# Performance work log

Hardware: AMD Instinct MI355X
Metric: run time of the kernel (lower is better)

## Reference

```python
import jax, jax.numpy as jnp
import numpy as np

EPS = 0.3
LAYERS = 2


def setup_inputs() -> dict:
    key = jax.random.key(0)
    ks = jax.random.split(key, 8)
    N, F, H, C, E = 50000, 512, 128, 40, 800000

    def xavier(k, shape):
        fan_out, fan_in = shape[0], shape[-1]
        std = 1.414 * np.sqrt(2.0 / (fan_in + fan_out))
        return (jax.random.normal(k, shape, jnp.float32) * std).astype(jnp.float32)

    return {
        "x": jax.random.normal(ks[0], (N, F), jnp.float32),
        "t1_w": xavier(ks[1], (H, F)),
        "t1_b": jnp.zeros((H,), jnp.float32),
        "t2_w": xavier(ks[2], (C, H)),
        "t2_b": jnp.zeros((C,), jnp.float32),
        "gate_w": xavier(ks[3], (LAYERS, 2 * H)),  # Linear(2H,1) weight per layer
        "gate_b": jnp.zeros((LAYERS,), jnp.float32),
        "edge_index": jax.random.randint(ks[4], (2, E), 0, N, jnp.int32),
    }


def reference(x, t1_w, t1_b, t2_w, t2_b, gate_w, gate_b, edge_index):
    N = x.shape[0]
    H = t1_w.shape[0]
    row, col = edge_index[0], edge_index[1]  # source, target

    # norm_degree = degree(row).clamp(min=1) ** -0.5
    deg = jax.ops.segment_sum(jnp.ones_like(row, dtype=x.dtype), row, num_segments=N)
    nd = jnp.clip(deg, 1.0) ** -0.5  # [N]
    nd_r, nd_c = nd[row], nd[col]    # [E]

    # dropout is identity in eval mode
    h = jax.nn.relu(x @ t1_w.T + t1_b)  # [N,H]
    raw = h
    for l in range(LAYERS):
        h_src = h[row]  # x_j, [E,H]
        h_dst = h[col]  # [E,H]
        # gate(cat([h[row], h[col]])) == h_src @ W[:H] + h_dst @ W[H:] + b
        g = jnp.tanh(h_src @ gate_w[l, :H] + h_dst @ gate_w[l, H:] + gate_b[l])  # [E]
        norm = g * nd_r * nd_c  # [E]
        agg = jax.ops.segment_sum(norm[:, None] * h_src, col, num_segments=N)  # scatter-add at targets
        h = EPS * raw + agg
    out = h @ t2_w.T + t2_b  # [N,C]
    return jax.nn.log_softmax(out, axis=1)
```

## Files before the change

kernel.cpp:

```cpp
#include <hip/hip_runtime.h>
#include <math.h>

#define F_DIM 512
#define H_DIM 128
#define C_DIM 40
#define EPS_F 0.3f
#define NBLK 160

typedef float f32x4 __attribute__((ext_vector_type(4)));
typedef unsigned int u32x4 __attribute__((ext_vector_type(4)));
typedef __bf16 bf16x8 __attribute__((ext_vector_type(8)));
typedef unsigned long long u64;
typedef unsigned short ushort_t;

__device__ inline float bflo(unsigned t) { return __builtin_bit_cast(float, t << 16); }
__device__ inline float bfhi(unsigned t) { return __builtin_bit_cast(float, t & 0xffff0000u); }
__device__ inline unsigned short f2bf(float f) {
  unsigned u = __builtin_bit_cast(unsigned, f);
  u = (u + 0x7fffu + ((u >> 16) & 1u)) >> 16;
  return (unsigned short)u;
}
__device__ inline unsigned pack2bf(float a, float b) {
  unsigned ua = __builtin_bit_cast(unsigned, a);
  unsigned ub = __builtin_bit_cast(unsigned, b);
  ua = (ua + 0x7fffu + ((ua >> 16) & 1u)) >> 16;
  ub = (ub + 0x7fffu + ((ub >> 16) & 1u)) >> 16;
  return ua | (ub << 16);
}


__global__ __launch_bounds__(256) void part_count(const int* __restrict__ row,
    const int* __restrict__ col, int* __restrict__ blkhist, int E, int nbkt, int chunk) {
  __shared__ int ch[256], rh[256];
  int t = threadIdx.x, b = blockIdx.x;
  ch[t] = 0; rh[t] = 0;
  __syncthreads();
  int s = b * chunk, e = min(E, s + chunk);
  for (int i = s + t; i < e; i += 256) {
    atomicAdd(&ch[((unsigned)col[i]) >> 8], 1);
    atomicAdd(&rh[((unsigned)row[i]) >> 8], 1);
  }
  __syncthreads();
  if (t < nbkt) {
    blkhist[t * NBLK + b] = ch[t];
    blkhist[nbkt * NBLK + t * NBLK + b] = rh[t];
  }
}

__global__ __launch_bounds__(256) void scan_partial(const int* __restrict__ cnt,
    int* __restrict__ part, int M) {
  __shared__ int sd[256];
  int t = threadIdx.x;
  int i = blockIdx.x * 256 + t;
  sd[t] = (i < M) ? cnt[i] : 0;
  __syncthreads();
  for (int s = 128; s > 0; s >>= 1) {
    if (t < s) sd[t] += sd[t + s];
    __syncthreads();
  }
  if (t == 0) part[blockIdx.x] = sd[0];
}

__global__ __launch_bounds__(256) void scan_single(int* __restrict__ part, int P) {
  __shared__ int sd[256];
  int t = threadIdx.x;
  sd[t] = (t < P) ? part[t] : 0;
  __syncthreads();
  for (int off = 1; off < 256; off <<= 1) {
    int add = (t >= off) ? sd[t - off] : 0;
    __syncthreads();
    sd[t] += add;
    __syncthreads();
  }
  if (t < P) part[t] = (t == 0) ? 0 : sd[t - 1];
}

__global__ __launch_bounds__(256) void scan_apply(const int* __restrict__ cnt,
    const int* __restrict__ part, int* __restrict__ sc, int M) {
  __shared__ int sd[256];
  int t = threadIdx.x;
  int i = blockIdx.x * 256 + t;
  int v = (i < M) ? cnt[i] : 0;
  sd[t] = v;
  __syncthreads();
  for (int off = 1; off < 256; off <<= 1) {
    int add = (t >= off) ? sd[t - off] : 0;
    __syncthreads();
    sd[t] += add;
    __syncthreads();
  }
  if (i < M) {
    int excl = (t == 0) ? 0 : sd[t - 1];
    sc[i] = part[blockIdx.x] + excl;
  }
}

__global__ __launch_bounds__(256) void part_scatter(const int* __restrict__ row,
    const int* __restrict__ col, const int* __restrict__ sc,
    u64* __restrict__ colpart, int* __restrict__ rowpart, int E, int nbkt, int chunk) {
  __shared__ int cbase[256], rbase[256], coff[256], roff[256];
  int t = threadIdx.x, b = blockIdx.x;
  if (t < nbkt) {
    cbase[t] = sc[t * NBLK + b];
    rbase[t] = sc[nbkt * NBLK + t * NBLK + b] - E;
  }
  coff[t] = 0; roff[t] = 0;
  __syncthreads();
  int s = b * chunk, e = min(E, s + chunk);
  for (int i = s + t; i < e; i += 256) {
    unsigned c = (unsigned)col[i], r = (unsigned)row[i];
    int pc = cbase[c >> 8] + atomicAdd(&coff[c >> 8], 1);
    colpart[pc] = ((u64)r << 32) | (u64)c;
    int pr = rbase[r >> 8] + atomicAdd(&roff[r >> 8], 1);
    rowpart[pr] = (int)r;
  }
}

__global__ __launch_bounds__(256) void bucket_csr(const u64* __restrict__ colpart,
    const int* __restrict__ sc, int* __restrict__ col_ptr, int* __restrict__ csr_src,
    int N, int E, int nbkt) {
  __shared__ int cnt[256], ex[256], off[256];
  int t = threadIdx.x, bkt = blockIdx.x;
  int s = sc[bkt * NBLK];
  int e = sc[(bkt + 1) * NBLK];
  cnt[t] = 0; off[t] = 0;
  __syncthreads();
  for (int i = s + t; i < e; i += 256)
    atomicAdd(&cnt[(int)(colpart[i] & 255u)], 1);
  __syncthreads();
  ex[t] = cnt[t];
  __syncthreads();
  for (int o = 1; o < 256; o <<= 1) {
    int v = (t >= o) ? ex[t - o] : 0;
    __syncthreads();
    ex[t] += v;
    __syncthreads();
  }
  int excl = (t == 0) ? 0 : ex[t - 1];
  __syncthreads();
  ex[t] = excl;
  __syncthreads();
  int node = bkt * 256 + t;
  if (node < N) col_ptr[node] = s + ex[t];
  if (bkt == 0 && t == 0) col_ptr[N] = E;
  for (int i = s + t; i < e; i += 256) {
    u64 p = colpart[i];
    int lb = (int)(p & 255u);
    int dst = s + ex[lb] + atomicAdd(&off[lb], 1);
    csr_src[dst] = (int)(p >> 32);
  }
}

__global__ __launch_bounds__(256) void bucket_deg(const int* __restrict__ rowpart,
    const int* __restrict__ sc, float* __restrict__ nd, int N, int E, int nbkt) {
  __shared__ int cnt[256];
  int t = threadIdx.x, bkt = blockIdx.x;
  int s = sc[nbkt * NBLK + bkt * NBLK] - E;
  int e = (bkt < nbkt - 1) ? (sc[nbkt * NBLK + (bkt + 1) * NBLK] - E) : E;
  cnt[t] = 0;
  __syncthreads();
  for (int i = s + t; i < e; i += 256)
    atomicAdd(&cnt[rowpart[i] & 255], 1);
  __syncthreads();
  int node = bkt * 256 + t;
  if (node < N) {
    int d = cnt[t] < 1 ? 1 : cnt[t];
    nd[node] = 1.0f / sqrtf((float)d);
  }
}


__global__ __launch_bounds__(256) void gemm1_mfma(const float* __restrict__ x,
    const float* __restrict__ w, const float* __restrict__ b,
    ushort_t* __restrict__ hbf, int N) {
  __shared__ u32x4 AsBuf[512];
  __shared__ u32x4 BsBuf[1024];
  char* Asc = (char*)AsBuf;
  char* Bsc = (char*)BsBuf;

  int t = threadIdx.x;
  int lane = t & 63;
  int wid = t >> 6;
  int wm = wid >> 1;
  int wn = wid & 1;
  int m0 = blockIdx.x * 64;

  f32x4 acc[2][4];
#pragma unroll
  for (int i = 0; i < 2; ++i)
#pragma unroll
    for (int j = 0; j < 4; ++j) acc[i][j] = (f32x4){0.f, 0.f, 0.f, 0.f};

  float bias[4];
#pragma unroll
  for (int j = 0; j < 4; ++j) bias[j] = b[wn * 64 + j * 16 + (lane & 15)];

  for (int kk = 0; kk < F_DIM; kk += 64) {
#pragma unroll
    for (int q = 0; q < 2; ++q) {
      int c = q * 256 + t;
      int row = c >> 3, kc = c & 7;
      int gm = m0 + row;
      f32x4 v0 = {0.f, 0.f, 0.f, 0.f}, v1 = {0.f, 0.f, 0.f, 0.f};
      if (gm < N) {
        const float* src = &x[(size_t)gm * F_DIM + kk + kc * 8];
        v0 = *(const f32x4*)src;
        v1 = *(const f32x4*)(src + 4);
      }
      u32x4 pk;
      pk[0] = pack2bf(v0[0], v0[1]);
      pk[1] = pack2bf(v0[2], v0[3]);
      pk[2] = pack2bf(v1[0], v1[1]);
      pk[3] = pack2bf(v1[2], v1[3]);
      *(u32x4*)(Asc + row * 128 + ((kc ^ (row & 7)) << 4)) = pk;
    }
#pragma unroll
    for (int q = 0; q < 4; ++q) {
      int c = q * 256 + t;
      int row = c >> 3, kc = c & 7;
      const float* src = &w[(size_t)row * F_DIM + kk + kc * 8];
      f32x4 v0 = *(const f32x4*)src;
      f32x4 v1 = *(const f32x4*)(src + 4);
      u32x4 pk;
      pk[0] = pack2bf(v0[0], v0[1]);
      pk[1] = pack2bf(v0[2], v0[3]);
      pk[2] = pack2bf(v1[0], v1[1]);
      pk[3] = pack2bf(v1[2], v1[3]);
      *(u32x4*)(Bsc + row * 128 + ((kc ^ (row & 7)) << 4)) = pk;
    }
    __syncthreads();
#pragma unroll
    for (int kh = 0; kh < 2; ++kh) {
      bf16x8 af[2], bfr[4];
      int kc = kh * 4 + (lane >> 4);
#pragma unroll
      for (int i = 0; i < 2; ++i) {
        int row = wm * 32 + i * 16 + (lane & 15);
        af[i] = *(const bf16x8*)(Asc + row * 128 + ((kc ^ (row & 7)) << 4));
      }
#pragma unroll
      for (int j = 0; j < 4; ++j) {
        int row = wn * 64 + j * 16 + (lane & 15);
        bfr[j] = *(const bf16x8*)(Bsc + row * 128 + ((kc ^ (row & 7)) << 4));
      }
#pragma unroll
      for (int i = 0; i < 2; ++i)
#pragma unroll
        for (int j = 0; j < 4; ++j)
          acc[i][j] = __builtin_amdgcn_mfma_f32_16x16x32_bf16(af[i], bfr[j], acc[i][j], 0, 0, 0);
    }
    __syncthreads();
  }

#pragma unroll
  for (int i = 0; i < 2; ++i)
#pragma unroll
    for (int j = 0; j < 4; ++j) {
      int col = wn * 64 + j * 16 + (lane & 15);
      int rbase = m0 + wm * 32 + i * 16 + ((lane >> 4) * 4);
#pragma unroll
      for (int r = 0; r < 4; ++r) {
        int gr = rbase + r;
        if (gr < N) hbf[(size_t)gr * H_DIM + col] = f2bf(fmaxf(acc[i][j][r] + bias[j], 0.f));
      }
    }
}


__global__ __launch_bounds__(256) void gate_s(const ushort_t* __restrict__ hbf,
    const float* __restrict__ gwl, const float* __restrict__ gb, int layer,
    float* __restrict__ s1, float* __restrict__ s2, int N) {
  int wid = (blockIdx.x * 256 + threadIdx.x) >> 6;
  int lane = threadIdx.x & 63;
  if (wid >= N) return;
  unsigned tv = *(const unsigned*)&hbf[(size_t)wid * H_DIM + lane * 2];
  float hx = bflo(tv), hy = bfhi(tv);
  float2 g1 = *(const float2*)&gwl[lane * 2];
  float2 g2 = *(const float2*)&gwl[H_DIM + lane * 2];
  float p1 = hx * g1.x + hy * g1.y;
  float p2 = hx * g2.x + hy * g2.y;
  for (int off = 32; off > 0; off >>= 1) {
    p1 += __shfl_xor(p1, off);
    p2 += __shfl_xor(p2, off);
  }
  if (lane == 0) {
    s1[wid] = p1;
    s2[wid] = p2 + gb[layer];
  }
}


__global__ __launch_bounds__(256) void agg_kernel(const ushort_t* __restrict__ hbf,
    const ushort_t* __restrict__ rawbf, const float* __restrict__ s1,
    const float* __restrict__ s2pb, const float* __restrict__ nd,
    const int* __restrict__ col_ptr, const int* __restrict__ csr_src,
    ushort_t* __restrict__ houtbf, int N) {
  int wid = (blockIdx.x * 256 + threadIdx.x) >> 6;
  int lane = threadIdx.x & 63;
  if (wid >= N) return;
  int v = wid;
  int p0 = col_ptr[v], p1 = col_ptr[v + 1];
  float s2v = s2pb[v];
  float ndv = nd[v];
  float ax = 0.f, ay = 0.f;
  for (int base = p0; base < p1; base += 64) {
    int idx = base + lane;
    int u = 0;
    float cf = 0.f;
    if (idx < p1) {
      u = csr_src[idx];
      cf = tanhf(s1[u] + s2v) * nd[u] * ndv;
    }
    int cnt = p1 - base;
    if (cnt > 64) cnt = 64;
    int j = 0;
    for (; j + 4 <= cnt; j += 4) {
      int u0 = __shfl(u, j + 0), u1 = __shfl(u, j + 1);
      int u2 = __shfl(u, j + 2), u3 = __shfl(u, j + 3);
      float c0 = __shfl(cf, j + 0), c1 = __shfl(cf, j + 1);
      float c2 = __shfl(cf, j + 2), c3 = __shfl(cf, j + 3);
      unsigned t0 = *(const unsigned*)&hbf[(size_t)u0 * H_DIM + lane * 2];
      unsigned t1 = *(const unsigned*)&hbf[(size_t)u1 * H_DIM + lane * 2];
      unsigned t2 = *(const unsigned*)&hbf[(size_t)u2 * H_DIM + lane * 2];
      unsigned t3 = *(const unsigned*)&hbf[(size_t)u3 * H_DIM + lane * 2];
      ax += c0 * bflo(t0) + c1 * bflo(t1) + c2 * bflo(t2) + c3 * bflo(t3);
      ay += c0 * bfhi(t0) + c1 * bfhi(t1) + c2 * bfhi(t2) + c3 * bfhi(t3);
    }
    for (; j < cnt; ++j) {
      int uj = __shfl(u, j);
      float cj = __shfl(cf, j);
      unsigned tj = *(const unsigned*)&hbf[(size_t)uj * H_DIM + lane * 2];
      ax += cj * bflo(tj);
      ay += cj * bfhi(tj);
    }
  }
  unsigned rv = *(const unsigned*)&rawbf[(size_t)v * H_DIM + lane * 2];
  float ox = EPS_F * bflo(rv) + ax;
  float oy = EPS_F * bfhi(rv) + ay;
  *(unsigned*)&houtbf[(size_t)v * H_DIM + lane * 2] = pack2bf(ox, oy);
}


__global__ __launch_bounds__(256) void gemm2_lsm(const ushort_t* __restrict__ hbf,
    const float* __restrict__ w, const float* __restrict__ b,
    float* __restrict__ out, int N) {
  __shared__ float ws[C_DIM][129];
  __shared__ float bsh[C_DIM];
  __shared__ float hsm[4][H_DIM];
  int t = threadIdx.x;
  for (int i = t; i < C_DIM * H_DIM; i += 256) ws[i / H_DIM][i % H_DIM] = w[i];
  if (t < C_DIM) bsh[t] = b[t];
  __syncthreads();
  int wave = t >> 6, lane = t & 63;
  for (int vb = blockIdx.x * 4; vb < N; vb += gridDim.x * 4) {
    int v = vb + wave;
    bool act = v < N;
    if (act) {
      unsigned hv = *(const unsigned*)&hbf[(size_t)v * H_DIM + lane * 2];
      hsm[wave][lane * 2] = bflo(hv);
      hsm[wave][lane * 2 + 1] = bfhi(hv);
    }
    __syncthreads();
    float acc = 0.f;
    if (act && lane < C_DIM) {
#pragma unroll 8
      for (int k = 0; k < H_DIM; ++k)
        acc = fmaf(hsm[wave][k], ws[lane][k], acc);
      acc += bsh[lane];
    }
    float m = (lane < C_DIM) ? acc : -1e30f;
    for (int off = 32; off > 0; off >>= 1) m = fmaxf(m, __shfl_xor(m, off));
    float ex = (lane < C_DIM) ? expf(acc - m) : 0.f;
    float s = ex;
    for (int off = 32; off > 0; off >>= 1) s += __shfl_xor(s, off);
    float lse = m + logf(s);
    if (act && lane < C_DIM) out[(size_t)v * C_DIM + lane] = acc - lse;
    __syncthreads();
  }
}


extern "C" void kernel_launch(void* const* d_in, const int* in_sizes, int n_in,
                              void* d_out, int out_size, void* d_ws, size_t ws_size,
                              hipStream_t stream) {
  const float* x   = (const float*)d_in[0];
  const float* t1w = (const float*)d_in[1];
  const float* t1b = (const float*)d_in[2];
  const float* t2w = (const float*)d_in[3];
  const float* t2b = (const float*)d_in[4];
  const float* gw  = (const float*)d_in[5];
  const float* gb  = (const float*)d_in[6];
  const int*   ei  = (const int*)d_in[7];
  const int N = in_sizes[0] / F_DIM;
  const int E = in_sizes[7] / 2;
  float* out = (float*)d_out;

  char* p = (char*)d_ws;
  auto take = [&](size_t bytes) {
    char* r = p;
    p += (bytes + 255) & ~(size_t)255;
    return r;
  };
  ushort_t* h0 = (ushort_t*)take((size_t)N * H_DIM * 2);
  ushort_t* h1 = (ushort_t*)take((size_t)N * H_DIM * 2);
  ushort_t* h2 = (ushort_t*)take((size_t)N * H_DIM * 2);
  float* s1 = (float*)take((size_t)N * 4);
  float* s2 = (float*)take((size_t)N * 4);
  float* nd = (float*)take((size_t)N * 4);
  int* col_ptr = (int*)take((size_t)(N + 1) * 4);
  int* csr_src = (int*)take((size_t)E * 4);

  const int nbkt = (N + 255) >> 8;
  const int chunk = (E + NBLK - 1) / NBLK;
  const int M = 2 * nbkt * NBLK;
  const int scanblocks = (M + 255) / 256;

  int* blkhist = (int*)take((size_t)M * 4);
  int* sc      = (int*)take((size_t)M * 4);
  int* part    = (int*)take(256 * 4);
  u64* colpart = (u64*)take((size_t)E * 8);
  int* rowpart = (int*)take((size_t)E * 4);

  const int* row = ei;
  const int* col = ei + E;

  part_count<<<NBLK, 256, 0, stream>>>(row, col, blkhist, E, nbkt, chunk);
  scan_partial<<<scanblocks, 256, 0, stream>>>(blkhist, part, M);
  scan_single<<<1, 256, 0, stream>>>(part, scanblocks);
  scan_apply<<<scanblocks, 256, 0, stream>>>(blkhist, part, sc, M);
  part_scatter<<<NBLK, 256, 0, stream>>>(row, col, sc, colpart, rowpart, E, nbkt, chunk);
  bucket_csr<<<nbkt, 256, 0, stream>>>(colpart, sc, col_ptr, csr_src, N, E, nbkt);
  bucket_deg<<<nbkt, 256, 0, stream>>>(rowpart, sc, nd, N, E, nbkt);

  gemm1_mfma<<<(N + 63) / 64, 256, 0, stream>>>(x, t1w, t1b, h0, N);

  int nwb = (N + 3) / 4;
  gate_s<<<nwb, 256, 0, stream>>>(h0, gw + 0 * 2 * H_DIM, gb, 0, s1, s2, N);
  agg_kernel<<<nwb, 256, 0, stream>>>(h0, h0, s1, s2, nd, col_ptr, csr_src, h1, N);
  gate_s<<<nwb, 256, 0, stream>>>(h1, gw + 1 * 2 * H_DIM, gb, 1, s1, s2, N);
  agg_kernel<<<nwb, 256, 0, stream>>>(h1, h0, s1, s2, nd, col_ptr, csr_src, h2, N);

  gemm2_lsm<<<1024, 256, 0, stream>>>(h2, t2w, t2b, out, N);
}
```

Measured before the change: 218.4 us.

## Fuse CSR build scans, compact partitions, enlarge GEMM1 tile, fuse gate into aggregation

The three-kernel global scan goes away: each part_scatter block computes its own bucket offsets by scanning the block histogram redundantly. Partitions shrink to 32-bit col and 8-bit row entries, and the CSR and degree bucket kernels merge into one launch. GEMM1 now processes 128 rows per block with a larger A tile, and the second layer's gate scores are computed in the first aggregation kernel's epilogue so the second gate_s launch is dropped. The redundant per-block histogram scan adds work to every block, and packing the row as r<<8 in 32 bits assumes fewer than 2^24 nodes.

```diff
diff --git a/kernel.cpp b/kernel.cpp
--- a/kernel.cpp
+++ b/kernel.cpp
@@ -5,13 +5,13 @@
 #define H_DIM 128
 #define C_DIM 40
 #define EPS_F 0.3f
-#define NBLK 160
+#define NBLK 256
 
 typedef float f32x4 __attribute__((ext_vector_type(4)));
 typedef unsigned int u32x4 __attribute__((ext_vector_type(4)));
 typedef __bf16 bf16x8 __attribute__((ext_vector_type(8)));
-typedef unsigned long long u64;
 typedef unsigned short ushort_t;
+typedef unsigned char uchar_t;
 
 __device__ inline float bflo(unsigned t) { return __builtin_bit_cast(float, t << 16); }
 __device__ inline float bfhi(unsigned t) { return __builtin_bit_cast(float, t & 0xffff0000u); }
@@ -43,129 +43,111 @@
   __syncthreads();
   if (t < nbkt) {
     blkhist[t * NBLK + b] = ch[t];
-    blkhist[nbkt * NBLK + t * NBLK + b] = rh[t];
-  }
-}
-
-__global__ __launch_bounds__(256) void scan_partial(const int* __restrict__ cnt,
-    int* __restrict__ part, int M) {
-  __shared__ int sd[256];
-  int t = threadIdx.x;
-  int i = blockIdx.x * 256 + t;
-  sd[t] = (i < M) ? cnt[i] : 0;
-  __syncthreads();
-  for (int s = 128; s > 0; s >>= 1) {
-    if (t < s) sd[t] += sd[t + s];
-    __syncthreads();
-  }
-  if (t == 0) part[blockIdx.x] = sd[0];
-}
-
-__global__ __launch_bounds__(256) void scan_single(int* __restrict__ part, int P) {
-  __shared__ int sd[256];
-  int t = threadIdx.x;
-  sd[t] = (t < P) ? part[t] : 0;
+    blkhist[(nbkt + t) * NBLK + b] = rh[t];
+  }
+}
+
+__global__ __launch_bounds__(256) void part_scatter(const int* __restrict__ row,
+    const int* __restrict__ col, const int* __restrict__ blkhist,
+    int* __restrict__ bktbase, unsigned* __restrict__ colpart,
+    uchar_t* __restrict__ rowpart, int E, int nbkt, int chunk) {
+  __shared__ int sbase[400];
+  __shared__ int stot[400];
+  __shared__ int psum[256];
+  __shared__ int sc[400];
+  __shared__ int coff[400];
+  int t = threadIdx.x, b = blockIdx.x;
+  int nrows = 2 * nbkt;
+  for (int rr = t; rr < nrows; rr += 256) {
+    const int* rp = &blkhist[rr * NBLK];
+    int pre = 0, tot = 0;
+    for (int i = 0; i < NBLK; ++i) {
+      int v = rp[i];
+      pre += (i < b) ? v : 0;
+      tot += v;
+    }
+    sbase[rr] = pre; stot[rr] = tot;
+  }
+  __syncthreads();
+  int e0 = (2 * t     < nrows) ? stot[2 * t]     : 0;
+  int e1 = (2 * t + 1 < nrows) ? stot[2 * t + 1] : 0;
+  psum[t] = e0 + e1;
   __syncthreads();
   for (int off = 1; off < 256; off <<= 1) {
-    int add = (t >= off) ? sd[t - off] : 0;
-    __syncthreads();
-    sd[t] += add;
-    __syncthreads();
-  }
-  if (t < P) part[t] = (t == 0) ? 0 : sd[t - 1];
-}
-
-__global__ __launch_bounds__(256) void scan_apply(const int* __restrict__ cnt,
-    const int* __restrict__ part, int* __restrict__ sc, int M) {
-  __shared__ int sd[256];
-  int t = threadIdx.x;
-  int i = blockIdx.x * 256 + t;
-  int v = (i < M) ? cnt[i] : 0;
-  sd[t] = v;
-  __syncthreads();
-  for (int off = 1; off < 256; off <<= 1) {
-    int add = (t >= off) ? sd[t - off] : 0;
-    __syncthreads();
-    sd[t] += add;
-    __syncthreads();
-  }
-  if (i < M) {
-    int excl = (t == 0) ? 0 : sd[t - 1];
-    sc[i] = part[blockIdx.x] + excl;
-  }
-}
-
-__global__ __launch_bounds__(256) void part_scatter(const int* __restrict__ row,
-    const int* __restrict__ col, const int* __restrict__ sc,
-    u64* __restrict__ colpart, int* __restrict__ rowpart, int E, int nbkt, int chunk) {
-  __shared__ int cbase[256], rbase[256], coff[256], roff[256];
-  int t = threadIdx.x, b = blockIdx.x;
-  if (t < nbkt) {
-    cbase[t] = sc[t * NBLK + b];
-    rbase[t] = sc[nbkt * NBLK + t * NBLK + b] - E;
-  }
-  coff[t] = 0; roff[t] = 0;
+    int add = (t >= off) ? psum[t - off] : 0;
+    __syncthreads();
+    psum[t] += add;
+    __syncthreads();
+  }
+  int pex = (t == 0) ? 0 : psum[t - 1];
+  if (2 * t < nrows)     sc[2 * t]     = pex + sbase[2 * t];
+  if (2 * t + 1 < nrows) sc[2 * t + 1] = pex + e0 + sbase[2 * t + 1];
+  if (b == 0) {
+    if (2 * t < nrows)     bktbase[2 * t]     = pex;
+    if (2 * t + 1 < nrows) bktbase[2 * t + 1] = pex + e0;
+    if (t == 0) bktbase[nrows] = 2 * E;
+  }
+  for (int rr = t; rr < nrows; rr += 256) coff[rr] = 0;
   __syncthreads();
   int s = b * chunk, e = min(E, s + chunk);
   for (int i = s + t; i < e; i += 256) {
     unsigned c = (unsigned)col[i], r = (unsigned)row[i];
-    int pc = cbase[c >> 8] + atomicAdd(&coff[c >> 8], 1);
-    colpart[pc] = ((u64)r << 32) | (u64)c;
-    int pr = rbase[r >> 8] + atomicAdd(&roff[r >> 8], 1);
-    rowpart[pr] = (int)r;
-  }
-}
-
-__global__ __launch_bounds__(256) void bucket_csr(const u64* __restrict__ colpart,
-    const int* __restrict__ sc, int* __restrict__ col_ptr, int* __restrict__ csr_src,
+    int bc = (int)(c >> 8), br = (int)(r >> 8);
+    int pc = sc[bc] + atomicAdd(&coff[bc], 1);
+    colpart[pc] = (r << 8) | (c & 255u);
+    int pr = sc[nbkt + br] + atomicAdd(&coff[nbkt + br], 1) - E;
+    rowpart[pr] = (uchar_t)(r & 255u);
+  }
+}
+
+__global__ __launch_bounds__(256) void bucket_both(const unsigned* __restrict__ colpart,
+    const uchar_t* __restrict__ rowpart, const int* __restrict__ bktbase,
+    int* __restrict__ col_ptr, int* __restrict__ csr_src, float* __restrict__ nd,
     int N, int E, int nbkt) {
   __shared__ int cnt[256], ex[256], off[256];
-  int t = threadIdx.x, bkt = blockIdx.x;
-  int s = sc[bkt * NBLK];
-  int e = sc[(bkt + 1) * NBLK];
-  cnt[t] = 0; off[t] = 0;
-  __syncthreads();
-  for (int i = s + t; i < e; i += 256)
-    atomicAdd(&cnt[(int)(colpart[i] & 255u)], 1);
-  __syncthreads();
-  ex[t] = cnt[t];
-  __syncthreads();
-  for (int o = 1; o < 256; o <<= 1) {
-    int v = (t >= o) ? ex[t - o] : 0;
-    __syncthreads();
-    ex[t] += v;
-    __syncthreads();
-  }
-  int excl = (t == 0) ? 0 : ex[t - 1];
-  __syncthreads();
-  ex[t] = excl;
-  __syncthreads();
-  int node = bkt * 256 + t;
-  if (node < N) col_ptr[node] = s + ex[t];
-  if (bkt == 0 && t == 0) col_ptr[N] = E;
-  for (int i = s + t; i < e; i += 256) {
-    u64 p = colpart[i];
-    int lb = (int)(p & 255u);
-    int dst = s + ex[lb] + atomicAdd(&off[lb], 1);
-    csr_src[dst] = (int)(p >> 32);
-  }
-}
-
-__global__ __launch_bounds__(256) void bucket_deg(const int* __restrict__ rowpart,
-    const int* __restrict__ sc, float* __restrict__ nd, int N, int E, int nbkt) {
-  __shared__ int cnt[256];
-  int t = threadIdx.x, bkt = blockIdx.x;
-  int s = sc[nbkt * NBLK + bkt * NBLK] - E;
-  int e = (bkt < nbkt - 1) ? (sc[nbkt * NBLK + (bkt + 1) * NBLK] - E) : E;
-  cnt[t] = 0;
-  __syncthreads();
-  for (int i = s + t; i < e; i += 256)
-    atomicAdd(&cnt[rowpart[i] & 255], 1);
-  __syncthreads();
-  int node = bkt * 256 + t;
-  if (node < N) {
-    int d = cnt[t] < 1 ? 1 : cnt[t];
-    nd[node] = 1.0f / sqrtf((float)d);
+  int t = threadIdx.x, bb = blockIdx.x;
+  if (bb < nbkt) {
+    int bkt = bb;
+    int s = bktbase[bkt], e = bktbase[bkt + 1];
+    cnt[t] = 0; off[t] = 0;
+    __syncthreads();
+    for (int i = s + t; i < e; i += 256)
+      atomicAdd(&cnt[(int)(colpart[i] & 255u)], 1);
+    __syncthreads();
+    ex[t] = cnt[t];
+    __syncthreads();
+    for (int o = 1; o < 256; o <<= 1) {
+      int v = (t >= o) ? ex[t - o] : 0;
+      __syncthreads();
+      ex[t] += v;
+      __syncthreads();
+    }
+    int excl = (t == 0) ? 0 : ex[t - 1];
+    __syncthreads();
+    ex[t] = excl;
+    __syncthreads();
+    int node = bkt * 256 + t;
+    if (node < N) col_ptr[node] = s + ex[t];
+    if (bkt == 0 && t == 0) col_ptr[N] = E;
+    for (int i = s + t; i < e; i += 256) {
+      unsigned p = colpart[i];
+      int lb = (int)(p & 255u);
+      int dst = s + ex[lb] + atomicAdd(&off[lb], 1);
+      csr_src[dst] = (int)(p >> 8);
+    }
+  } else {
+    int bkt = bb - nbkt;
+    int s = bktbase[nbkt + bkt] - E, e = bktbase[nbkt + bkt + 1] - E;
+    cnt[t] = 0;
+    __syncthreads();
+    for (int i = s + t; i < e; i += 256)
+      atomicAdd(&cnt[(int)rowpart[i]], 1);
+    __syncthreads();
+    int node = bkt * 256 + t;
+    if (node < N) {
+      int d = cnt[t] < 1 ? 1 : cnt[t];
+      nd[node] = 1.0f / sqrtf((float)d);
+    }
   }
 }
 
@@ -173,7 +155,7 @@
 __global__ __launch_bounds__(256) void gemm1_mfma(const float* __restrict__ x,
     const float* __restrict__ w, const float* __restrict__ b,
     ushort_t* __restrict__ hbf, int N) {
-  __shared__ u32x4 AsBuf[512];
+  __shared__ u32x4 AsBuf[1024];
   __shared__ u32x4 BsBuf[1024];
   char* Asc = (char*)AsBuf;
   char* Bsc = (char*)BsBuf;
@@ -183,11 +165,11 @@
   int wid = t >> 6;
   int wm = wid >> 1;
   int wn = wid & 1;
-  int m0 = blockIdx.x * 64;
-
-  f32x4 acc[2][4];
-#pragma unroll
-  for (int i = 0; i < 2; ++i)
+  int m0 = blockIdx.x * 128;
+
+  f32x4 acc[4][4];
+#pragma unroll
+  for (int i = 0; i < 4; ++i)
 #pragma unroll
     for (int j = 0; j < 4; ++j) acc[i][j] = (f32x4){0.f, 0.f, 0.f, 0.f};
 
@@ -197,7 +179,7 @@
 
   for (int kk = 0; kk < F_DIM; kk += 64) {
 #pragma unroll
-    for (int q = 0; q < 2; ++q) {
+    for (int q = 0; q < 4; ++q) {
       int c = q * 256 + t;
       int row = c >> 3, kc = c & 7;
       int gm = m0 + row;
@@ -231,11 +213,11 @@
     __syncthreads();
 #pragma unroll
     for (int kh = 0; kh < 2; ++kh) {
-      bf16x8 af[2], bfr[4];
+      bf16x8 af[4], bfr[4];
       int kc = kh * 4 + (lane >> 4);
 #pragma unroll
-      for (int i = 0; i < 2; ++i) {
-        int row = wm * 32 + i * 16 + (lane & 15);
+      for (int i = 0; i < 4; ++i) {
+        int row = wm * 64 + i * 16 + (lane & 15);
         af[i] = *(const bf16x8*)(Asc + row * 128 + ((kc ^ (row & 7)) << 4));
       }
 #pragma unroll
@@ -244,7 +226,7 @@
         bfr[j] = *(const bf16x8*)(Bsc + row * 128 + ((kc ^ (row & 7)) << 4));
       }
 #pragma unroll
-      for (int i = 0; i < 2; ++i)
+      for (int i = 0; i < 4; ++i)
 #pragma unroll
         for (int j = 0; j < 4; ++j)
           acc[i][j] = __builtin_amdgcn_mfma_f32_16x16x32_bf16(af[i], bfr[j], acc[i][j], 0, 0, 0);
@@ -253,11 +235,11 @@
   }
 
 #pragma unroll
-  for (int i = 0; i < 2; ++i)
+  for (int i = 0; i < 4; ++i)
 #pragma unroll
     for (int j = 0; j < 4; ++j) {
       int col = wn * 64 + j * 16 + (lane & 15);
-      int rbase = m0 + wm * 32 + i * 16 + ((lane >> 4) * 4);
+      int rbase = m0 + wm * 64 + i * 16 + ((lane >> 4) * 4);
 #pragma unroll
       for (int r = 0; r < 4; ++r) {
         int gr = rbase + r;
@@ -290,11 +272,14 @@
 }
 
 
+template <bool GATE>
 __global__ __launch_bounds__(256) void agg_kernel(const ushort_t* __restrict__ hbf,
     const ushort_t* __restrict__ rawbf, const float* __restrict__ s1,
     const float* __restrict__ s2pb, const float* __restrict__ nd,
     const int* __restrict__ col_ptr, const int* __restrict__ csr_src,
-    ushort_t* __restrict__ houtbf, int N) {
+    ushort_t* __restrict__ houtbf,
+    const float* __restrict__ gwl, const float* __restrict__ gb, int layer,
+    float* __restrict__ s1o, float* __restrict__ s2o, int N) {
   int wid = (blockIdx.x * 256 + threadIdx.x) >> 6;
   int lane = threadIdx.x & 63;
   if (wid >= N) return;
@@ -338,6 +323,20 @@
   float ox = EPS_F * bflo(rv) + ax;
   float oy = EPS_F * bfhi(rv) + ay;
   *(unsigned*)&houtbf[(size_t)v * H_DIM + lane * 2] = pack2bf(ox, oy);
+  if (GATE) {
+    float2 g1 = *(const float2*)&gwl[lane * 2];
+    float2 g2 = *(const float2*)&gwl[H_DIM + lane * 2];
+    float q1 = ox * g1.x + oy * g1.y;
+    float q2 = ox * g2.x + oy * g2.y;
+    for (int off = 32; off > 0; off >>= 1) {
+      q1 += __shfl_xor(q1, off);
+      q2 += __shfl_xor(q2, off);
+    }
+    if (lane == 0) {
+      s1o[v] = q1;
+      s2o[v] = q2 + gb[layer];
+    }
+  }
 }
 
 
@@ -404,41 +403,37 @@
   ushort_t* h0 = (ushort_t*)take((size_t)N * H_DIM * 2);
   ushort_t* h1 = (ushort_t*)take((size_t)N * H_DIM * 2);
   ushort_t* h2 = (ushort_t*)take((size_t)N * H_DIM * 2);
-  float* s1 = (float*)take((size_t)N * 4);
-  float* s2 = (float*)take((size_t)N * 4);
-  float* nd = (float*)take((size_t)N * 4);
+  float* s1a = (float*)take((size_t)N * 4);
+  float* s2a = (float*)take((size_t)N * 4);
+  float* s1b = (float*)take((size_t)N * 4);
+  float* s2b = (float*)take((size_t)N * 4);
+  float* nd  = (float*)take((size_t)N * 4);
   int* col_ptr = (int*)take((size_t)(N + 1) * 4);
   int* csr_src = (int*)take((size_t)E * 4);
 
   const int nbkt = (N + 255) >> 8;
   const int chunk = (E + NBLK - 1) / NBLK;
-  const int M = 2 * nbkt * NBLK;
-  const int scanblocks = (M + 255) / 256;
-
-  int* blkhist = (int*)take((size_t)M * 4);
-  int* sc      = (int*)take((size_t)M * 4);
-  int* part    = (int*)take(256 * 4);
-  u64* colpart = (u64*)take((size_t)E * 8);
-  int* rowpart = (int*)take((size_t)E * 4);
+
+  int* blkhist = (int*)take((size_t)2 * nbkt * NBLK * 4);
+  int* bktbase = (int*)take((size_t)(2 * nbkt + 1) * 4);
+  unsigned* colpart = (unsigned*)take((size_t)E * 4);
+  uchar_t* rowpart  = (uchar_t*)take((size_t)E);
 
   const int* row = ei;
   const int* col = ei + E;
 
+  gemm1_mfma<<<(N + 127) / 128, 256, 0, stream>>>(x, t1w, t1b, h0, N);
+
   part_count<<<NBLK, 256, 0, stream>>>(row, col, blkhist, E, nbkt, chunk);
-  scan_partial<<<scanblocks, 256, 0, stream>>>(blkhist, part, M);
-  scan_single<<<1, 256, 0, stream>>>(part, scanblocks);
-  scan_apply<<<scanblocks, 256, 0, stream>>>(blkhist, part, sc, M);
-  part_scatter<<<NBLK, 256, 0, stream>>>(row, col, sc, colpart, rowpart, E, nbkt, chunk);
-  bucket_csr<<<nbkt, 256, 0, stream>>>(colpart, sc, col_ptr, csr_src, N, E, nbkt);
-  bucket_deg<<<nbkt, 256, 0, stream>>>(rowpart, sc, nd, N, E, nbkt);
-
-  gemm1_mfma<<<(N + 63) / 64, 256, 0, stream>>>(x, t1w, t1b, h0, N);
+  part_scatter<<<NBLK, 256, 0, stream>>>(row, col, blkhist, bktbase, colpart, rowpart, E, nbkt, chunk);
+  bucket_both<<<2 * nbkt, 256, 0, stream>>>(colpart, rowpart, bktbase, col_ptr, csr_src, nd, N, E, nbkt);
 
   int nwb = (N + 3) / 4;
-  gate_s<<<nwb, 256, 0, stream>>>(h0, gw + 0 * 2 * H_DIM, gb, 0, s1, s2, N);
-  agg_kernel<<<nwb, 256, 0, stream>>>(h0, h0, s1, s2, nd, col_ptr, csr_src, h1, N);
-  gate_s<<<nwb, 256, 0, stream>>>(h1, gw + 1 * 2 * H_DIM, gb, 1, s1, s2, N);
-  agg_kernel<<<nwb, 256, 0, stream>>>(h1, h0, s1, s2, nd, col_ptr, csr_src, h2, N);
+  gate_s<<<nwb, 256, 0, stream>>>(h0, gw + 0 * 2 * H_DIM, gb, 0, s1a, s2a, N);
+  agg_kernel<true><<<nwb, 256, 0, stream>>>(h0, h0, s1a, s2a, nd, col_ptr, csr_src, h1,
+                                            gw + 1 * 2 * H_DIM, gb, 1, s1b, s2b, N);
+  agg_kernel<false><<<nwb, 256, 0, stream>>>(h1, h0, s1b, s2b, nd, col_ptr, csr_src, h2,
+                                             nullptr, nullptr, 0, nullptr, nullptr, N);
 
   gemm2_lsm<<<1024, 256, 0, stream>>>(h2, t2w, t2b, out, N);
 }
```

Measured after the change: 210.8 us. -3.5%, faster.
